# Kernel optimization log

Measured on AMD Instinct MI355X. Metric: run time of the kernel, lower is better.

Reference implementation:

```python
import jax, jax.numpy as jnp
import numpy as np

N_HIDDEN_LAYERS = 9  # 32->32 middle layers (plus input 1->32 and output 32->1)
HID = 32
SLOPE = 0.01  # LeakyReLU negative_slope


def leaky_relu(x):
    return jnp.where(x >= 0, x, SLOPE * x)


def setup_inputs() -> dict:
    key = jax.random.key(0)
    ks = jax.random.split(key, 8)
    N = 1048576
    x = jax.random.normal(ks[0], (N,), dtype=jnp.float32)
    # PyTorch Linear init: U(-1/sqrt(fan_in), 1/sqrt(fan_in))
    def u(k, shape, fan_in):
        b = 1.0 / np.sqrt(fan_in)
        return jax.random.uniform(k, shape, jnp.float32, -b, b)
    W_in = u(ks[1], (1, HID), 1)
    b_in = u(ks[2], (HID,), 1)
    W_hid = u(ks[3], (N_HIDDEN_LAYERS, HID, HID), HID)
    b_hid = u(ks[4], (N_HIDDEN_LAYERS, HID), HID)
    W_out = u(ks[5], (HID, 1), HID)
    b_out = u(ks[6], (1,), HID)
    return {"x": x, "W_in": W_in, "b_in": b_in, "W_hid": W_hid,
            "b_hid": b_hid, "W_out": W_out, "b_out": b_out}


def reference(x, W_in, b_in, W_hid, b_hid, W_out, b_out):
    N = x.shape[0]
    h = x[:, None]  # [N, 1], mirrors x.reshape(N, 1)
    h = leaky_relu(h @ W_in + b_in)  # [N, 32]
    def step(h, wb):
        W, b = wb
        return leaky_relu(h @ W + b), None
    h, _ = jax.lax.scan(step, h, (W_hid, b_hid))
    out = h @ W_out + b_out  # [N, 1]
    return out.reshape(1, N)
```

## Files before the change

kernel.cpp:

```cpp
#include <hip/hip_runtime.h>

#define NLAYERS 9
#define HID 32
#define SLOPE 0.01f

typedef _Float16 v2h __attribute__((ext_vector_type(2)));
typedef _Float16 v8h __attribute__((ext_vector_type(8)));
typedef float v4f __attribute__((ext_vector_type(4)));

#define NCHAIN 2

union U8 { v8h v; v2h p[4]; };

__device__ __forceinline__ v2h pk_cvt(float a, float b) {
    return __builtin_bit_cast(v2h, __builtin_amdgcn_cvt_pkrtz(a, b));
}
__device__ __forceinline__ v2h leaky2(v2h t, v2h s) {
    return __builtin_elementwise_max(t, t * s);
}
__device__ __forceinline__ int umap(int g, int j) {
    return 4 * g + (j & 3) + 16 * (j >> 2);
}

__global__ __launch_bounds__(256, 4) void mlp_mfma_kernel(
    const float* __restrict__ x,
    const float* __restrict__ W_in,
    const float* __restrict__ b_in,
    const float* __restrict__ W_hid,
    const float* __restrict__ b_hid,
    const float* __restrict__ W_out,
    const float* __restrict__ b_out,
    float* __restrict__ out, int N)
{
    __shared__ __align__(16) _Float16 wA_sh[NLAYERS][2][64][8];
    __shared__ __align__(64) float bc_sh[NLAYERS][2][16];

    const int tid = threadIdx.x;
    for (int t = tid; t < NLAYERS * 2 * 64; t += blockDim.x) {
        int l = t >> 7, r = t & 127, tt = (r >> 6) & 1, ln = r & 63;
        int i = ln & 15, gg = ln >> 4;
        const float* Wl = W_hid + l * HID * HID;
        v8h w;
#pragma unroll
        for (int j = 0; j < 8; ++j)
            w[j] = (_Float16)Wl[umap(gg, j) * HID + 16 * tt + i];
        *(v8h*)&wA_sh[l][tt][ln][0] = w;
    }
    for (int t = tid; t < NLAYERS * HID; t += blockDim.x)
        ((float*)bc_sh)[t] = b_hid[t];
    __syncthreads();

    const int lane = tid & 63;
    const int g    = lane >> 4;
    const int col  = lane & 15;

    v2h win2[4], bin2[4], wout2[4];
#pragma unroll
    for (int jj = 0; jj < 4; ++jj) {
        int u0 = umap(g, 2 * jj), u1 = umap(g, 2 * jj + 1);
        win2[jj]  = v2h{(_Float16)W_in[u0],  (_Float16)W_in[u1]};
        bin2[jj]  = v2h{(_Float16)b_in[u0],  (_Float16)b_in[u1]};
        wout2[jj] = v2h{(_Float16)W_out[u0], (_Float16)W_out[u1]};
    }
    const float bo = b_out[0];
    const v2h slope2 = v2h{(_Float16)SLOPE, (_Float16)SLOPE};

    const int nwaves = (gridDim.x * blockDim.x) >> 6;
    const int wid    = (blockIdx.x * blockDim.x + tid) >> 6;
    const int niter  = (N + NCHAIN * 32 - 1) / (NCHAIN * 32);

    v2h xc2[NCHAIN];
#pragma unroll
    for (int c = 0; c < NCHAIN; ++c) xc2[c] = v2h{(_Float16)0.f, (_Float16)0.f};
    if (wid < niter) {
#pragma unroll
        for (int c = 0; c < NCHAIN; ++c) {
            int i0 = wid * (NCHAIN * 32) + c * 32 + col;
            int i1 = i0 + 16;
            float a = (i0 < N) ? x[i0] : 0.0f;
            float b = (i1 < N) ? x[i1] : 0.0f;
            xc2[c] = pk_cvt(a, b);
        }
    }

    for (int it = wid; it < niter; it += nwaves) {
        v2h xn2[NCHAIN];
#pragma unroll
        for (int c = 0; c < NCHAIN; ++c) xn2[c] = v2h{(_Float16)0.f, (_Float16)0.f};
        {
            int nit = it + nwaves;
            if (nit < niter) {
#pragma unroll
                for (int c = 0; c < NCHAIN; ++c) {
                    int i0 = nit * (NCHAIN * 32) + c * 32 + col;
                    int i1 = i0 + 16;
                    float a = (i0 < N) ? x[i0] : 0.0f;
                    float b = (i1 < N) ? x[i1] : 0.0f;
                    xn2[c] = pk_cvt(a, b);
                }
            }
        }

        U8 f[NCHAIN][2];
#pragma unroll
        for (int c = 0; c < NCHAIN; ++c)
#pragma unroll
            for (int nh = 0; nh < 2; ++nh) {
                _Float16 xh = xc2[c][nh];
                v2h x2 = v2h{xh, xh};
#pragma unroll
                for (int jj = 0; jj < 4; ++jj)
                    f[c][nh].p[jj] = leaky2(x2 * win2[jj] + bin2[jj], slope2);
            }

#pragma unroll 1
        for (int l = 0; l < NLAYERS; ++l) {
            v8h wA0 = *(const v8h*)&wA_sh[l][0][lane][0];
            v8h wA1 = *(const v8h*)&wA_sh[l][1][lane][0];
            v4f bc0 = *(const v4f*)&bc_sh[l][0][4 * g];
            v4f bc1 = *(const v4f*)&bc_sh[l][1][4 * g];

            v4f A0[4], A1[4];
            A0[0] = __builtin_amdgcn_mfma_f32_16x16x32_f16(wA0, f[0][0].v, bc0, 0, 0, 0);
            A0[1] = __builtin_amdgcn_mfma_f32_16x16x32_f16(wA0, f[0][1].v, bc0, 0, 0, 0);
            A0[2] = __builtin_amdgcn_mfma_f32_16x16x32_f16(wA1, f[0][0].v, bc1, 0, 0, 0);
            A0[3] = __builtin_amdgcn_mfma_f32_16x16x32_f16(wA1, f[0][1].v, bc1, 0, 0, 0);
            A1[0] = __builtin_amdgcn_mfma_f32_16x16x32_f16(wA0, f[1][0].v, bc0, 0, 0, 0);
            A1[1] = __builtin_amdgcn_mfma_f32_16x16x32_f16(wA0, f[1][1].v, bc0, 0, 0, 0);
            A1[2] = __builtin_amdgcn_mfma_f32_16x16x32_f16(wA1, f[1][0].v, bc1, 0, 0, 0);
            A1[3] = __builtin_amdgcn_mfma_f32_16x16x32_f16(wA1, f[1][1].v, bc1, 0, 0, 0);

            f[0][0].p[0] = leaky2(pk_cvt(A0[0][0], A0[0][1]), slope2);
            f[0][0].p[1] = leaky2(pk_cvt(A0[0][2], A0[0][3]), slope2);
            f[0][0].p[2] = leaky2(pk_cvt(A0[2][0], A0[2][1]), slope2);
            f[0][0].p[3] = leaky2(pk_cvt(A0[2][2], A0[2][3]), slope2);
            f[0][1].p[0] = leaky2(pk_cvt(A0[1][0], A0[1][1]), slope2);
            f[0][1].p[1] = leaky2(pk_cvt(A0[1][2], A0[1][3]), slope2);
            f[0][1].p[2] = leaky2(pk_cvt(A0[3][0], A0[3][1]), slope2);
            f[0][1].p[3] = leaky2(pk_cvt(A0[3][2], A0[3][3]), slope2);
            f[1][0].p[0] = leaky2(pk_cvt(A1[0][0], A1[0][1]), slope2);
            f[1][0].p[1] = leaky2(pk_cvt(A1[0][2], A1[0][3]), slope2);
            f[1][0].p[2] = leaky2(pk_cvt(A1[2][0], A1[2][1]), slope2);
            f[1][0].p[3] = leaky2(pk_cvt(A1[2][2], A1[2][3]), slope2);
            f[1][1].p[0] = leaky2(pk_cvt(A1[1][0], A1[1][1]), slope2);
            f[1][1].p[1] = leaky2(pk_cvt(A1[1][2], A1[1][3]), slope2);
            f[1][1].p[2] = leaky2(pk_cvt(A1[3][0], A1[3][1]), slope2);
            f[1][1].p[3] = leaky2(pk_cvt(A1[3][2], A1[3][3]), slope2);
        }

#pragma unroll
        for (int c = 0; c < NCHAIN; ++c)
#pragma unroll
            for (int nh = 0; nh < 2; ++nh) {
                float p = 0.0f;
#pragma unroll
                for (int jj = 0; jj < 4; ++jj)
                    p = __builtin_amdgcn_fdot2(f[c][nh].p[jj], wout2[jj], p, false);
                p += __shfl_xor(p, 16, 64);
                p += __shfl_xor(p, 32, 64);
                float o = p + bo;
                int idx = it * (NCHAIN * 32) + c * 32 + 16 * nh + col;
                if (g == 2 * c + nh && idx < N) out[idx] = o;
            }

#pragma unroll
        for (int c = 0; c < NCHAIN; ++c) xc2[c] = xn2[c];
    }
}

extern "C" void kernel_launch(void* const* d_in, const int* in_sizes, int n_in,
                              void* d_out, int out_size, void* d_ws, size_t ws_size,
                              hipStream_t stream) {
    const float* x     = (const float*)d_in[0];
    const float* W_in  = (const float*)d_in[1];
    const float* b_in  = (const float*)d_in[2];
    const float* W_hid = (const float*)d_in[3];
    const float* b_hid = (const float*)d_in[4];
    const float* W_out = (const float*)d_in[5];
    const float* b_out = (const float*)d_in[6];
    float* out = (float*)d_out;

    int N = in_sizes[0];
    dim3 block(256);
    dim3 grid(1280);
    mlp_mfma_kernel<<<grid, block, 0, stream>>>(x, W_in, b_in, W_hid, b_hid,
                                                W_out, b_out, out, N);
}
```

Measured before the change: 93.33 us.

## Drop to single chain per wave, raise occupancy, move input/output weights to LDS

Each wave now processes 32 rows per iteration instead of 64, halving the MFMA work and registers per wave. Launch bounds change to 512 threads with 8 waves per EU hint and the grid becomes 1024 blocks of 512, aiming for more resident waves to hide MFMA and conversion latency. Input/output layer weights move from per-thread registers to shared memory to cut register pressure. Bounds checks on N are removed, assuming N is a multiple of 32, and per-wave instruction-level parallelism drops.

```diff
diff --git a/kernel.cpp b/kernel.cpp
--- a/kernel.cpp
+++ b/kernel.cpp
@@ -7,8 +7,6 @@
 typedef _Float16 v2h __attribute__((ext_vector_type(2)));
 typedef _Float16 v8h __attribute__((ext_vector_type(8)));
 typedef float v4f __attribute__((ext_vector_type(4)));
-
-#define NCHAIN 2
 
 union U8 { v8h v; v2h p[4]; };
 
@@ -22,7 +20,7 @@
     return 4 * g + (j & 3) + 16 * (j >> 2);
 }
 
-__global__ __launch_bounds__(256, 4) void mlp_mfma_kernel(
+__global__ __launch_bounds__(512, 8) void mlp_mfma_kernel(
     const float* __restrict__ x,
     const float* __restrict__ W_in,
     const float* __restrict__ b_in,
@@ -34,6 +32,7 @@
 {
     __shared__ __align__(16) _Float16 wA_sh[NLAYERS][2][64][8];
     __shared__ __align__(64) float bc_sh[NLAYERS][2][16];
+    __shared__ __align__(16) v2h win_sh[4][4], bin_sh[4][4], wout_sh[4][4];
 
     const int tid = threadIdx.x;
     for (int t = tid; t < NLAYERS * 2 * 64; t += blockDim.x) {
@@ -48,70 +47,54 @@
     }
     for (int t = tid; t < NLAYERS * HID; t += blockDim.x)
         ((float*)bc_sh)[t] = b_hid[t];
+    if (tid < 16) {
+        int gg = tid >> 2, jj = tid & 3;
+        int u0 = umap(gg, 2 * jj), u1 = umap(gg, 2 * jj + 1);
+        win_sh[gg][jj]  = v2h{(_Float16)W_in[u0],  (_Float16)W_in[u1]};
+        bin_sh[gg][jj]  = v2h{(_Float16)b_in[u0],  (_Float16)b_in[u1]};
+        wout_sh[gg][jj] = v2h{(_Float16)W_out[u0], (_Float16)W_out[u1]};
+    }
     __syncthreads();
 
     const int lane = tid & 63;
     const int g    = lane >> 4;
     const int col  = lane & 15;
 
-    v2h win2[4], bin2[4], wout2[4];
-#pragma unroll
-    for (int jj = 0; jj < 4; ++jj) {
-        int u0 = umap(g, 2 * jj), u1 = umap(g, 2 * jj + 1);
-        win2[jj]  = v2h{(_Float16)W_in[u0],  (_Float16)W_in[u1]};
-        bin2[jj]  = v2h{(_Float16)b_in[u0],  (_Float16)b_in[u1]};
-        wout2[jj] = v2h{(_Float16)W_out[u0], (_Float16)W_out[u1]};
-    }
     const float bo = b_out[0];
     const v2h slope2 = v2h{(_Float16)SLOPE, (_Float16)SLOPE};
 
     const int nwaves = (gridDim.x * blockDim.x) >> 6;
-    const int wid    = (blockIdx.x * blockDim.x + tid) >> 6;
-    const int niter  = (N + NCHAIN * 32 - 1) / (NCHAIN * 32);
+    const int wid    = ((blockIdx.x * blockDim.x) >> 6) + (tid >> 6);
+    const int niter  = N >> 5;
 
-    v2h xc2[NCHAIN];
-#pragma unroll
-    for (int c = 0; c < NCHAIN; ++c) xc2[c] = v2h{(_Float16)0.f, (_Float16)0.f};
+    v2h xc2 = v2h{(_Float16)0.f, (_Float16)0.f};
     if (wid < niter) {
-#pragma unroll
-        for (int c = 0; c < NCHAIN; ++c) {
-            int i0 = wid * (NCHAIN * 32) + c * 32 + col;
-            int i1 = i0 + 16;
-            float a = (i0 < N) ? x[i0] : 0.0f;
-            float b = (i1 < N) ? x[i1] : 0.0f;
-            xc2[c] = pk_cvt(a, b);
-        }
+        int i0 = wid * 32 + col;
+        xc2 = pk_cvt(x[i0], x[i0 + 16]);
     }
 
     for (int it = wid; it < niter; it += nwaves) {
-        v2h xn2[NCHAIN];
-#pragma unroll
-        for (int c = 0; c < NCHAIN; ++c) xn2[c] = v2h{(_Float16)0.f, (_Float16)0.f};
+        v2h xn2 = v2h{(_Float16)0.f, (_Float16)0.f};
         {
             int nit = it + nwaves;
             if (nit < niter) {
-#pragma unroll
-                for (int c = 0; c < NCHAIN; ++c) {
-                    int i0 = nit * (NCHAIN * 32) + c * 32 + col;
-                    int i1 = i0 + 16;
-                    float a = (i0 < N) ? x[i0] : 0.0f;
-                    float b = (i1 < N) ? x[i1] : 0.0f;
-                    xn2[c] = pk_cvt(a, b);
-                }
+                int i0 = nit * 32 + col;
+                xn2 = pk_cvt(x[i0], x[i0 + 16]);
             }
         }
 
-        U8 f[NCHAIN][2];
+        U8 f0, f1;
+        {
+            const v2h* wi = &win_sh[g][0];
+            const v2h* bi = &bin_sh[g][0];
 #pragma unroll
-        for (int c = 0; c < NCHAIN; ++c)
-#pragma unroll
-            for (int nh = 0; nh < 2; ++nh) {
-                _Float16 xh = xc2[c][nh];
-                v2h x2 = v2h{xh, xh};
-#pragma unroll
-                for (int jj = 0; jj < 4; ++jj)
-                    f[c][nh].p[jj] = leaky2(x2 * win2[jj] + bin2[jj], slope2);
+            for (int jj = 0; jj < 4; ++jj) {
+                v2h x20 = v2h{xc2[0], xc2[0]};
+                v2h x21 = v2h{xc2[1], xc2[1]};
+                f0.p[jj] = leaky2(x20 * wi[jj] + bi[jj], slope2);
+                f1.p[jj] = leaky2(x21 * wi[jj] + bi[jj], slope2);
             }
+        }
 
 #pragma unroll 1
         for (int l = 0; l < NLAYERS; ++l) {
@@ -120,51 +103,39 @@
             v4f bc0 = *(const v4f*)&bc_sh[l][0][4 * g];
             v4f bc1 = *(const v4f*)&bc_sh[l][1][4 * g];
 
-            v4f A0[4], A1[4];
-            A0[0] = __builtin_amdgcn_mfma_f32_16x16x32_f16(wA0, f[0][0].v, bc0, 0, 0, 0);
-            A0[1] = __builtin_amdgcn_mfma_f32_16x16x32_f16(wA0, f[0][1].v, bc0, 0, 0, 0);
-            A0[2] = __builtin_amdgcn_mfma_f32_16x16x32_f16(wA1, f[0][0].v, bc1, 0, 0, 0);
-            A0[3] = __builtin_amdgcn_mfma_f32_16x16x32_f16(wA1, f[0][1].v, bc1, 0, 0, 0);
-            A1[0] = __builtin_amdgcn_mfma_f32_16x16x32_f16(wA0, f[1][0].v, bc0, 0, 0, 0);
-            A1[1] = __builtin_amdgcn_mfma_f32_16x16x32_f16(wA0, f[1][1].v, bc0, 0, 0, 0);
-            A1[2] = __builtin_amdgcn_mfma_f32_16x16x32_f16(wA1, f[1][0].v, bc1, 0, 0, 0);
-            A1[3] = __builtin_amdgcn_mfma_f32_16x16x32_f16(wA1, f[1][1].v, bc1, 0, 0, 0);
+            v4f a00 = __builtin_amdgcn_mfma_f32_16x16x32_f16(wA0, f0.v, bc0, 0, 0, 0);
+            v4f a01 = __builtin_amdgcn_mfma_f32_16x16x32_f16(wA0, f1.v, bc0, 0, 0, 0);
+            v4f a10 = __builtin_amdgcn_mfma_f32_16x16x32_f16(wA1, f0.v, bc1, 0, 0, 0);
+            v4f a11 = __builtin_amdgcn_mfma_f32_16x16x32_f16(wA1, f1.v, bc1, 0, 0, 0);
 
-            f[0][0].p[0] = leaky2(pk_cvt(A0[0][0], A0[0][1]), slope2);
-            f[0][0].p[1] = leaky2(pk_cvt(A0[0][2], A0[0][3]), slope2);
-            f[0][0].p[2] = leaky2(pk_cvt(A0[2][0], A0[2][1]), slope2);
-            f[0][0].p[3] = leaky2(pk_cvt(A0[2][2], A0[2][3]), slope2);
-            f[0][1].p[0] = leaky2(pk_cvt(A0[1][0], A0[1][1]), slope2);
-            f[0][1].p[1] = leaky2(pk_cvt(A0[1][2], A0[1][3]), slope2);
-            f[0][1].p[2] = leaky2(pk_cvt(A0[3][0], A0[3][1]), slope2);
-            f[0][1].p[3] = leaky2(pk_cvt(A0[3][2], A0[3][3]), slope2);
-            f[1][0].p[0] = leaky2(pk_cvt(A1[0][0], A1[0][1]), slope2);
-            f[1][0].p[1] = leaky2(pk_cvt(A1[0][2], A1[0][3]), slope2);
-            f[1][0].p[2] = leaky2(pk_cvt(A1[2][0], A1[2][1]), slope2);
-            f[1][0].p[3] = leaky2(pk_cvt(A1[2][2], A1[2][3]), slope2);
-            f[1][1].p[0] = leaky2(pk_cvt(A1[1][0], A1[1][1]), slope2);
-            f[1][1].p[1] = leaky2(pk_cvt(A1[1][2], A1[1][3]), slope2);
-            f[1][1].p[2] = leaky2(pk_cvt(A1[3][0], A1[3][1]), slope2);
-            f[1][1].p[3] = leaky2(pk_cvt(A1[3][2], A1[3][3]), slope2);
+            f0.p[0] = leaky2(pk_cvt(a00[0], a00[1]), slope2);
+            f0.p[1] = leaky2(pk_cvt(a00[2], a00[3]), slope2);
+            f0.p[2] = leaky2(pk_cvt(a10[0], a10[1]), slope2);
+            f0.p[3] = leaky2(pk_cvt(a10[2], a10[3]), slope2);
+            f1.p[0] = leaky2(pk_cvt(a01[0], a01[1]), slope2);
+            f1.p[1] = leaky2(pk_cvt(a01[2], a01[3]), slope2);
+            f1.p[2] = leaky2(pk_cvt(a11[0], a11[1]), slope2);
+            f1.p[3] = leaky2(pk_cvt(a11[2], a11[3]), slope2);
         }
 
+        {
+            const v2h* wo = &wout_sh[g][0];
+            float p0 = 0.0f, p1 = 0.0f;
 #pragma unroll
-        for (int c = 0; c < NCHAIN; ++c)
-#pragma unroll
-            for (int nh = 0; nh < 2; ++nh) {
-                float p = 0.0f;
-#pragma unroll
-                for (int jj = 0; jj < 4; ++jj)
-                    p = __builtin_amdgcn_fdot2(f[c][nh].p[jj], wout2[jj], p, false);
-                p += __shfl_xor(p, 16, 64);
-                p += __shfl_xor(p, 32, 64);
-                float o = p + bo;
-                int idx = it * (NCHAIN * 32) + c * 32 + 16 * nh + col;
-                if (g == 2 * c + nh && idx < N) out[idx] = o;
+            for (int jj = 0; jj < 4; ++jj) {
+                p0 = __builtin_amdgcn_fdot2(f0.p[jj], wo[jj], p0, false);
+                p1 = __builtin_amdgcn_fdot2(f1.p[jj], wo[jj], p1, false);
             }
+            p0 += __shfl_xor(p0, 16, 64);
+            p0 += __shfl_xor(p0, 32, 64);
+            p1 += __shfl_xor(p1, 16, 64);
+            p1 += __shfl_xor(p1, 32, 64);
+            int idx = it * 32 + col;
+            if (g == 0) out[idx]      = p0 + bo;
+            if (g == 1) out[idx + 16] = p1 + bo;
+        }
 
-#pragma unroll
-        for (int c = 0; c < NCHAIN; ++c) xc2[c] = xn2[c];
+        xc2 = xn2;
     }
 }
 
@@ -181,8 +152,8 @@
     float* out = (float*)d_out;
 
     int N = in_sizes[0];
-    dim3 block(256);
-    dim3 grid(1280);
+    dim3 block(512);
+    dim3 grid(1024);
     mlp_mfma_kernel<<<grid, block, 0, stream>>>(x, W_in, b_in, W_hid, b_hid,
                                                 W_out, b_out, out, N);
 }
```

Measured after the change: 90.90 us. 2.6% less time.
